# Optimization experiments

Measured on AMD Instinct MI355X. Metric: run time of the kernel, lower is better.

Reference implementation:

```python
import jax, jax.numpy as jnp
import numpy as np

B, T, S, D, V, L = 32, 128, 256, 1024, 10000, 2
EOS = 2


def setup_inputs() -> dict:
    key = jax.random.key(0)
    ks = jax.random.split(key, 12)
    s = 0.02
    targets = jax.random.randint(ks[0], (B, T), 0, V)
    targets = jnp.where(targets == EOS, 3, targets)  # decoder strips eos; keep rectangular
    return {
        'encoder_outputs': jax.random.normal(ks[1], (B, S, D), jnp.float32),
        'targets': targets,
        'emb': jax.random.normal(ks[2], (V, D)) * s,
        'W_ih': jax.random.normal(ks[3], (L, 4 * D, D)) * s,
        'W_hh': jax.random.normal(ks[4], (L, 4 * D, D)) * s,
        'b_ih': jnp.zeros((L, 4 * D)),
        'b_hh': jnp.zeros((L, 4 * D)),
        'Wconv': jax.random.normal(ks[5], (D, 3)) * s,   # Conv1d(1 -> attn_dim, k=3) kernel
        'bconv': jnp.zeros((D,)),
        'Wq': jax.random.normal(ks[6], (D, D)) * s,      # query_proj (no bias)
        'Wv': jax.random.normal(ks[7], (D, D)) * s,      # value_proj (no bias)
        'attn_bias': jax.random.uniform(ks[8], (D,), minval=-0.1, maxval=0.1),
        'fc_attn_w': jax.random.normal(ks[9], (D,)) * s, # attention score fc (D -> 1)
        'fc_attn_b': jnp.zeros(()),
        'fc1_w': jax.random.normal(ks[10], (D, 2 * D)) * s,  # Linear(2D -> D)
        'fc1_b': jnp.zeros((D,)),
        'fc2_w': jax.random.normal(ks[11], (V, D)) * s,      # Linear(D -> V)
        'fc2_b': jnp.zeros((V,)),
    }


def _forward(encoder_outputs, targets, emb, W_ih, W_hh, b_ih, b_hh, Wconv, bconv,
             Wq, Wv, attn_bias, fc_attn_w, fc_attn_b, fc1_w, fc1_b, fc2_w, fc2_b):
    b, s_len = encoder_outputs.shape[0], encoder_outputs.shape[1]
    # value_proj(encoder_outputs) is constant across decode steps
    vproj = jnp.einsum('bsd,ed->bse', encoder_outputs, Wv)
    embedded = emb[targets]                  # (B,T,D)
    xs = jnp.swapaxes(embedded, 0, 1)        # (T,B,D)
    h0 = jnp.zeros((L, b, D), embedded.dtype)
    c0 = jnp.zeros((L, b, D), embedded.dtype)
    a0 = jnp.zeros((b, s_len), embedded.dtype)  # last alignment energy starts at zero

    def step(carry, x_t):
        h, c, attn = carry
        inp = x_t
        hs, cs = [], []
        for l in range(L):  # fixed small number of LSTM layers
            gates = inp @ W_ih[l].T + b_ih[l] + h[l] @ W_hh[l].T + b_hh[l]
            i, f, g, o = jnp.split(gates, 4, axis=-1)
            c_l = jax.nn.sigmoid(f) * c[l] + jax.nn.sigmoid(i) * jnp.tanh(g)
            h_l = jax.nn.sigmoid(o) * jnp.tanh(c_l)
            hs.append(h_l); cs.append(c_l); inp = h_l
        q = inp  # decoder rnn output for this step, (B,D)
        # location_conv: Conv1d(1->D, k=3, pad=1) over last alignment
        pad = jnp.pad(attn, ((0, 0), (1, 1)))
        win = jnp.stack([pad[:, :-2], pad[:, 1:-1], pad[:, 2:]], axis=-1)  # (B,S,3)
        loc = jnp.einsum('bsk,dk->bsd', win, Wconv) + bconv
        qp = q @ Wq.T
        e = jnp.tanh(qp[:, None, :] + vproj + loc + attn_bias)  # (B,S,D)
        energy = jnp.einsum('bsd,d->bs', e, fc_attn_w) + fc_attn_b
        new_attn = jax.nn.softmax(energy, axis=-1)
        context = jnp.einsum('bs,bsd->bd', new_attn, encoder_outputs)
        hid = jnp.tanh(jnp.concatenate([q, context], axis=-1) @ fc1_w.T + fc1_b)
        logp = jax.nn.log_softmax(hid @ fc2_w.T + fc2_b, axis=-1)
        return (jnp.stack(hs), jnp.stack(cs), new_attn), logp

    _, logps = jax.lax.scan(step, (h0, c0, a0), xs)  # (T,B,V)
    return jnp.swapaxes(logps, 0, 1)                 # (B,T,V) log-probs


def reference(encoder_outputs, targets, emb, W_ih, W_hh, b_ih, b_hh, Wconv, bconv,
              Wq, Wv, attn_bias, fc_attn_w, fc_attn_b, fc1_w, fc1_b, fc2_w, fc2_b):
    return _forward(encoder_outputs, targets, emb, W_ih, W_hh, b_ih, b_hh, Wconv, bconv,
                    Wq, Wv, attn_bias, fc_attn_w, fc_attn_b, fc1_w, fc1_b, fc2_w, fc2_b)
```

## Files before the change

### kernel.cpp

```cpp
#include <hip/hip_runtime.h>
#include <stdint.h>

#define B_ 32
#define T_ 128
#define S_ 256
#define D_ 1024
#define V_ 10000

typedef unsigned short u16;
typedef unsigned char u8;
typedef unsigned long long u64;
typedef __attribute__((ext_vector_type(8))) short bf16x8;
typedef __attribute__((ext_vector_type(4))) float f32x4;
typedef __attribute__((ext_vector_type(4))) unsigned int u32x4;

__device__ __forceinline__ float bf2f(u16 u){ union { unsigned int i; float f; } v; v.i = ((unsigned int)u)<<16; return v.f; }
__device__ __forceinline__ u16 f2bf(float f){ union { float ff; unsigned int i; } v; v.ff = f; unsigned int x = v.i; return (u16)((x + 0x7fffu + ((x>>16)&1u))>>16); }
__device__ __forceinline__ float fp82f(unsigned int x){
  union { unsigned int i; float f; } v;
  v.i = ((x & 0x80u) << 24) | ((x & 0x7Fu) << 20);
  return v.f * 0x1.0p+120f;
}
__device__ __forceinline__ u8 f2fp8(float f){
  union { float ff; unsigned int i; } v;
  v.ff = fminf(fmaxf(f, -240.f), 240.f) * 0x1.0p-120f;
  unsigned int s = (v.i >> 24) & 0x80u;
  unsigned int u = v.i & 0x7FFFFFFFu;
  u += ((u >> 20) & 1u) + 0x7FFFFu;
  return (u8)(s | ((u >> 20) & 0x7Fu));
}
__device__ __forceinline__ float ftanh(float x){
  float e = __expf(2.f*x);
  return __builtin_fmaf(-2.f, __builtin_amdgcn_rcpf(1.f+e), 1.f);
}
__device__ __forceinline__ float sigm(float x){
  return __builtin_amdgcn_rcpf(1.f + __expf(-x));
}

__global__ void k_cast(const float* __restrict__ in, u16* __restrict__ out, long n){
  for (long i = (long)blockIdx.x*blockDim.x + threadIdx.x; i < n; i += (long)gridDim.x*blockDim.x)
    out[i] = f2bf(in[i]);
}

__global__ void k_cast8(const float* __restrict__ in, u8* __restrict__ out, long n){
  for (long i = (long)blockIdx.x*blockDim.x + threadIdx.x; i < n; i += (long)gridDim.x*blockDim.x)
    out[i] = f2fp8(in[i]);
}

__global__ void k_w1cat(const float* __restrict__ wih1, const float* __restrict__ whh1, u16* __restrict__ out){
  const long n = (long)4096*2048;
  for (long i = (long)blockIdx.x*blockDim.x + threadIdx.x; i < n; i += (long)gridDim.x*blockDim.x){
    int row = (int)(i >> 11), k = (int)(i & 2047);
    float v = (k < D_) ? wih1[(size_t)row*D_ + k] : whh1[(size_t)row*D_ + (k - D_)];
    out[i] = f2bf(v);
  }
}

__global__ void k_bias(const float* __restrict__ bih, const float* __restrict__ bhh,
                       const float* __restrict__ bcv, const float* __restrict__ abias,
                       const float* __restrict__ Wcv, const float* __restrict__ fcw,
                       float* __restrict__ bias0, float* __restrict__ bias1,
                       float* __restrict__ biasE, float* __restrict__ convw){
  int i = blockIdx.x*blockDim.x + threadIdx.x;
  if (i < 4096){ bias0[i] = bih[i]+bhh[i]; bias1[i] = bih[4096+i]+bhh[4096+i]; }
  if (i < 1024){
    biasE[i] = bcv[i]+abias[i];
    convw[i*4+0]=Wcv[i*3+0]; convw[i*4+1]=Wcv[i*3+1]; convw[i*4+2]=Wcv[i*3+2]; convw[i*4+3]=fcw[i];
  }
}

__global__ void k_gather(const float* __restrict__ emb, const int* __restrict__ tgt, u16* __restrict__ embA){
  int row = blockIdx.x;
  int t = row >> 5, b = row & 31;
  int e = tgt[b*T_ + t];
  const float* src = emb + (size_t)e*D_;
  u16* dst = embA + (size_t)row*D_;
  for (int d = threadIdx.x; d < D_; d += 256) dst[d] = f2bf(src[d]);
}

__device__ __forceinline__ void gld_lds(const u16* g, u16* l){
  __builtin_amdgcn_global_load_lds((const __attribute__((address_space(1))) unsigned int*)g,
                                   (__attribute__((address_space(3))) unsigned int*)l, 16, 0, 0);
}

template<int OUT_MODE, bool SWIZ>
__global__ __launch_bounds__(256) void k_gemm128(const u16* __restrict__ Am, const u16* __restrict__ Bm,
      const float* __restrict__ bias, void* __restrict__ Cout, int M, int N, int K, int lda, int ldc)
{
  __shared__ u16 As[128*32];
  __shared__ u16 Bs[128*32];
  int bm = blockIdx.y*128, bn = blockIdx.x*128;
  int tid = threadIdx.x;
  int wv = tid>>6, lane = tid&63;
  int wm = (wv>>1)*64, wn = (wv&1)*64;
  int r = lane&15, kh = lane>>4;
  f32x4 zero = {0.f,0.f,0.f,0.f};
  f32x4 acc[4][4];
  #pragma unroll
  for (int mi=0;mi<4;mi++)
    #pragma unroll
    for (int ni=0;ni<4;ni++) acc[mi][ni] = zero;

  for (int k0 = 0; k0 < K; k0 += 32){
    #pragma unroll
    for (int i=0;i<2;i++){
      int c = tid + i*256;
      int row = c>>2, ko = (c&3)*8;
      int ga = bm+row; if (ga > M-1) ga = M-1;
      gld_lds(Am + (size_t)ga*lda + k0 + ko, As + c*8);
      int gb = bn+row; if (gb > N-1) gb = N-1;
      gld_lds(Bm + (size_t)gb*K + k0 + ko, Bs + c*8);
    }
    __syncthreads();
    bf16x8 af[4], bfv[4];
    #pragma unroll
    for (int mi=0;mi<4;mi++) af[mi]  = *(const bf16x8*)(As + (wm+mi*16+r)*32 + kh*8);
    #pragma unroll
    for (int ni=0;ni<4;ni++) bfv[ni] = *(const bf16x8*)(Bs + (wn+ni*16+r)*32 + kh*8);
    #pragma unroll
    for (int mi=0;mi<4;mi++)
      #pragma unroll
      for (int ni=0;ni<4;ni++)
        acc[mi][ni] = __builtin_amdgcn_mfma_f32_16x16x32_bf16(af[mi], bfv[ni], acc[mi][ni], 0,0,0);
    __syncthreads();
  }
  #pragma unroll
  for (int mi=0;mi<4;mi++)
    #pragma unroll
    for (int ni=0;ni<4;ni++)
      #pragma unroll
      for (int rr=0;rr<4;rr++){
        int grow = bm+wm+mi*16+kh*4+rr;
        int gcol = bn+wn+ni*16+r;
        if (grow < M && gcol < N){
          float v = acc[mi][ni][rr];
          if (bias) v += bias[gcol];
          size_t orow = SWIZ ? (size_t)((grow&31)*T_ + (grow>>5)) : (size_t)grow;
          if (OUT_MODE==0)      ((float*)Cout)[orow*(size_t)ldc + gcol] = v;
          else if (OUT_MODE==1) ((u16*)Cout)[orow*(size_t)ldc + gcol] = f2bf(v);
          else if (OUT_MODE==2) ((u16*)Cout)[orow*(size_t)ldc + gcol] = f2bf(ftanh(v));
          else                  ((u8*)Cout)[orow*(size_t)ldc + gcol] = f2fp8(v);
        }
      }
}

__device__ __forceinline__ void xcd_barrier(int* barL, int it){
  asm volatile("s_waitcnt vmcnt(0)" ::: "memory");
  __syncthreads();
  if (threadIdx.x==0){
    int grp = blockIdx.x & 7;
    int* gcnt = barL + grp*32;
    int* root = barL + 256;
    int* rel  = barL + 320 + grp*32;
    int v = __hip_atomic_fetch_add(gcnt, 1, __ATOMIC_RELAXED, __HIP_MEMORY_SCOPE_AGENT);
    if (v == 32*(it+1) - 1){
      int rv = __hip_atomic_fetch_add(root, 1, __ATOMIC_RELAXED, __HIP_MEMORY_SCOPE_AGENT);
      if (rv == 8*(it+1) - 1){
        #pragma unroll
        for (int g2=0; g2<8; ++g2)
          __hip_atomic_store(barL + 320 + g2*32, it+1, __ATOMIC_RELAXED, __HIP_MEMORY_SCOPE_AGENT);
      }
    }
    while (__hip_atomic_load(rel, __ATOMIC_RELAXED, __HIP_MEMORY_SCOPE_AGENT) < it+1)
      __builtin_amdgcn_s_sleep(2);
  }
  __syncthreads();
}

__global__ __launch_bounds__(512) void k_fused(const u16* __restrict__ Whh0, const u16* __restrict__ W1cat,
    const u16* __restrict__ Wqm, const u16* __restrict__ X0, const float* __restrict__ bias1,
    const u8* __restrict__ vp8, const u8* __restrict__ enc8, const float* __restrict__ convw,
    u16* __restrict__ Hh, u16* __restrict__ qps, float* __restrict__ eng,
    u16* __restrict__ qcat, int* __restrict__ barL)
{
  __shared__ u16 W0s[16*1024];
  __shared__ u16 W1s[16*2048];
  __shared__ u16 Wqs[4*1024];
  __shared__ float gl0[8*512];
  __shared__ float gl1[8*512];
  __shared__ float glq[4*128];
  __shared__ float aw[256];
  __shared__ float red[16];
  __shared__ float cred[512];
  __shared__ u16 hb0[128];
  __shared__ u16 hb1[128];
  __shared__ u16 hbq[128];
  int bid = blockIdx.x, tid = threadIdx.x;
  int w = tid>>6, lane = tid&63, r = lane&15, kh = lane>>4;
  int batt = bid>>3, part = bid&7;
  int d0 = lane*16;
  for (int ci = tid; ci < 2048; ci += 512){
    int row = ci>>7, c = ci&127;
    int grow = (row>>2)*1024 + bid*4 + (row&3);
    bf16x8 v = *(const bf16x8*)(Whh0 + (size_t)grow*1024 + c*8);
    *(bf16x8*)(W0s + (size_t)(((row<<7) + (c ^ (row&7)))*8)) = v;
  }
  for (int ci = tid; ci < 4096; ci += 512){
    int row = ci>>8, c = ci&255;
    int grow = (row>>2)*1024 + bid*4 + (row&3);
    bf16x8 v = *(const bf16x8*)(W1cat + (size_t)grow*2048 + c*8);
    *(bf16x8*)(W1s + (size_t)(((row<<8) + (c ^ (row&7)))*8)) = v;
  }
  {
    int row = tid>>7, c = tid&127;
    bf16x8 v = *(const bf16x8*)(Wqm + (size_t)(bid*4+row)*1024 + c*8);
    *(bf16x8*)(Wqs + (size_t)(((row<<7) + (c ^ (row&7)))*8)) = v;
  }
  if (tid < 256) aw[tid] = 0.f;
  __syncthreads();
  float c0reg = 0.f, c1reg = 0.f;
  int cb = tid>>2, cj = tid&3;
  int col = bid*4 + cj;
  float b1i=0.f, b1f=0.f, b1g=0.f, b1o=0.f;
  if (tid < 128){ b1i=bias1[col]; b1f=bias1[1024+col]; b1g=bias1[2048+col]; b1o=bias1[3072+col]; }
  for (int i = 0; i <= T_+3; ++i){
    const u16* Hprev = Hh + (size_t)i*65536;
    u16* Hcur = (u16*)Hh + (size_t)(i+1)*65536;
    bool doG0 = (i < T_);
    bool doG1 = (i >= 1 && i <= T_);
    bool loadG1 = (i >= 1 && i <= T_+1);
    bool doQP = (i >= 2 && i <= T_+1);
    bool doEN = (i >= 3 && i <= T_+2);
    bool doSM = (i >= 4);
    float x_gi=0.f, x_gf=0.f, x_gg=0.f, x_go=0.f;
    if (doG0 && tid < 128){
      const u16* xr = X0 + ((size_t)i*32 + cb)*4096 + col;
      x_gi = bf2f(xr[0]); x_gf = bf2f(xr[1024]); x_gg = bf2f(xr[2048]); x_go = bf2f(xr[3072]);
    }
    bf16x8 a_g0[2][4], a_g1[2][8];
    if (doG0){
      const u16* a0 = Hprev + (size_t)r*2048 + w*128 + kh*8;
      const u16* a1 = Hprev + (size_t)(16+r)*2048 + w*128 + kh*8;
      #pragma unroll
      for (int kk=0;kk<4;kk++){ a_g0[0][kk] = *(const bf16x8*)(a0 + kk*32);
                                a_g0[1][kk] = *(const bf16x8*)(a1 + kk*32); }
    }
    if (loadG1){
      const u16* a0 = Hprev + (size_t)r*2048 + w*256 + kh*8;
      const u16* a1 = Hprev + (size_t)(16+r)*2048 + w*256 + kh*8;
      #pragma unroll
      for (int kk=0;kk<8;kk++){ a_g1[0][kk] = *(const bf16x8*)(a0 + kk*32);
                                a_g1[1][kk] = *(const bf16x8*)(a1 + kk*32); }
    }
    if (doSM){
      int t = i-4;
      float* ebuf = eng + (t&1)*8192 + batt*256;
      float e_val = -3.0e38f;
      if (tid < 256)
        e_val = __hip_atomic_load(ebuf + tid, __ATOMIC_RELAXED, __HIP_MEMORY_SCOPE_AGENT);
      float m = e_val;
      #pragma unroll
      for (int o=32;o;o>>=1) m = fmaxf(m, __shfl_xor(m,o));
      if (lane==0) red[w] = m;
      __syncthreads();
      float mx = red[0];
      #pragma unroll
      for (int i2=1;i2<8;i2++) mx = fmaxf(mx, red[i2]);
      float ex = (tid < 256) ? __expf(e_val - mx) : 0.f;
      float sl = ex;
      #pragma unroll
      for (int o=32;o;o>>=1) sl += __shfl_xor(sl,o);
      __syncthreads();
      if (lane==0) red[8+w] = sl;
      __syncthreads();
      float st = red[8]+red[9]+red[10]+red[11]+red[12]+red[13]+red[14]+red[15];
      if (tid < 256) aw[tid] = ex * __builtin_amdgcn_rcpf(st);
      __syncthreads();
      int sq = tid>>7, dt = tid&127;
      const u8* ep = enc8 + (size_t)(batt*256 + sq*64)*1024 + part*128 + dt;
      float a0=0.f,a1=0.f,a2=0.f,a3=0.f;
      #pragma unroll 4
      for (int s2=0;s2<64;s2+=4){
        a0 += aw[sq*64+s2]   * fp82f(ep[(size_t)(s2)  *1024]);
        a1 += aw[sq*64+s2+1] * fp82f(ep[(size_t)(s2+1)*1024]);
        a2 += aw[sq*64+s2+2] * fp82f(ep[(size_t)(s2+2)*1024]);
        a3 += aw[sq*64+s2+3] * fp82f(ep[(size_t)(s2+3)*1024]);
      }
      cred[tid] = a0+a1+a2+a3;
      __syncthreads();
      if (tid < 128)
        qcat[((size_t)t*32 + batt)*2048 + 1024 + part*128 + tid] =
          f2bf(cred[tid]+cred[128+tid]+cred[256+tid]+cred[384+tid]);
    }
    f32x4 acc00={0.f,0.f,0.f,0.f}, acc01={0.f,0.f,0.f,0.f};
    f32x4 acc10={0.f,0.f,0.f,0.f}, acc11={0.f,0.f,0.f,0.f};
    f32x4 accq0={0.f,0.f,0.f,0.f}, accq1={0.f,0.f,0.f,0.f};
    if (doG0){
      #pragma unroll
      for (int kk=0;kk<4;kk++){
        int c = (w<<4) + (kk<<2) + kh;
        bf16x8 bv = *(const bf16x8*)(W0s + (size_t)((((int)r<<7) + (c ^ (r&7)))*8));
        acc00 = __builtin_amdgcn_mfma_f32_16x16x32_bf16(a_g0[0][kk], bv, acc00, 0,0,0);
        acc01 = __builtin_amdgcn_mfma_f32_16x16x32_bf16(a_g0[1][kk], bv, acc01, 0,0,0);
      }
    }
    if (doG1){
      #pragma unroll
      for (int kk=0;kk<8;kk++){
        int c = (w<<5) + (kk<<2) + kh;
        bf16x8 bv = *(const bf16x8*)(W1s + (size_t)((((int)r<<8) + (c ^ (r&7)))*8));
        acc10 = __builtin_amdgcn_mfma_f32_16x16x32_bf16(a_g1[0][kk], bv, acc10, 0,0,0);
        acc11 = __builtin_amdgcn_mfma_f32_16x16x32_bf16(a_g1[1][kk], bv, acc11, 0,0,0);
      }
    }
    if (doQP && w >= 4){
      #pragma unroll
      for (int kk=0;kk<8;kk++){
        int c = ((w-4)<<5) + (kk<<2) + kh;
        int qrw = r & 3;
        bf16x8 bv = *(const bf16x8*)(Wqs + (size_t)(((qrw<<7) + (c ^ (qrw&7)))*8));
        accq0 = __builtin_amdgcn_mfma_f32_16x16x32_bf16(a_g1[0][kk], bv, accq0, 0,0,0);
        accq1 = __builtin_amdgcn_mfma_f32_16x16x32_bf16(a_g1[1][kk], bv, accq1, 0,0,0);
      }
    }
    #pragma unroll
    for (int rr=0;rr<4;rr++){
      gl0[w*512 + (kh*4+rr)*16 + r]    = acc00[rr];
      gl0[w*512 + (16+kh*4+rr)*16 + r] = acc01[rr];
      gl1[w*512 + (kh*4+rr)*16 + r]    = acc10[rr];
      gl1[w*512 + (16+kh*4+rr)*16 + r] = acc11[rr];
    }
    if (doQP && w >= 4 && r < 4){
      #pragma unroll
      for (int rr=0;rr<4;rr++){
        glq[(w-4)*128 + (kh*4+rr)*4 + r]      = accq0[rr];
        glq[(w-4)*128 + (16+kh*4+rr)*4 + r]   = accq1[rr];
      }
    }
    __syncthreads();
    if (tid < 128){
      if (doG0){
        float gi=x_gi, gf=x_gf, gg=x_gg, go=x_go;
        #pragma unroll
        for (int ww=0;ww<8;ww++){
          const float* gp = gl0 + ww*512 + cb*16 + cj;
          gi += gp[0]; gf += gp[4]; gg += gp[8]; go += gp[12];
        }
        float cn = sigm(gf)*c0reg + sigm(gi)*ftanh(gg);
        float hn = sigm(go)*ftanh(cn); c0reg = cn;
        hb0[tid] = f2bf(hn);
      }
      if (doG1){
        float gi=b1i, gf=b1f, gg=b1g, go=b1o;
        #pragma unroll
        for (int ww=0;ww<8;ww++){
          const float* gp = gl1 + ww*512 + cb*16 + cj;
          gi += gp[0]; gf += gp[4]; gg += gp[8]; go += gp[12];
        }
        float cn = sigm(gf)*c1reg + sigm(gi)*ftanh(gg);
        float hn = sigm(go)*ftanh(cn); c1reg = cn;
        hb1[tid] = f2bf(hn);
      }
      if (doQP)
        hbq[tid] = f2bf(glq[tid] + glq[128+tid] + glq[256+tid] + glq[384+tid]);
    }
    __syncthreads();
    if (tid < 32){
      union { u64 v; u16 s[4]; } pk;
      if (doG0){
        pk.s[0]=hb0[tid*4]; pk.s[1]=hb0[tid*4+1]; pk.s[2]=hb0[tid*4+2]; pk.s[3]=hb0[tid*4+3];
        __hip_atomic_store((u64*)(Hcur + (size_t)tid*2048 + bid*4), pk.v,
                           __ATOMIC_RELAXED, __HIP_MEMORY_SCOPE_AGENT);
      }
      if (doG1){
        pk.s[0]=hb1[tid*4]; pk.s[1]=hb1[tid*4+1]; pk.s[2]=hb1[tid*4+2]; pk.s[3]=hb1[tid*4+3];
        __hip_atomic_store((u64*)(Hcur + (size_t)tid*2048 + 1024 + bid*4), pk.v,
                           __ATOMIC_RELAXED, __HIP_MEMORY_SCOPE_AGENT);
        *(u64*)(qcat + ((size_t)(i-1)*32 + tid)*2048 + bid*4) = pk.v;
      }
      if (doQP){
        pk.s[0]=hbq[tid*4]; pk.s[1]=hbq[tid*4+1]; pk.s[2]=hbq[tid*4+2]; pk.s[3]=hbq[tid*4+3];
        __hip_atomic_store((u64*)(qps + ((size_t)(i-2)*32 + tid)*1024 + bid*4), pk.v,
                           __ATOMIC_RELAXED, __HIP_MEMORY_SCOPE_AGENT);
      }
    }
    if (doEN){
      int t = i-3;
      float* ebuf = eng + (t&1)*8192 + batt*256;
      const u16* qrow = qps + ((size_t)t*32 + batt)*1024 + d0;
      bf16x8 q0 = *(const bf16x8*)qrow, q1 = *(const bf16x8*)(qrow+8);
      float qf[16];
      #pragma unroll
      for (int j=0;j<16;j++) qf[j] = bf2f((u16)(j<8 ? q0[j] : q1[j-8]));
      f32x4 cw[16];
      #pragma unroll
      for (int j=0;j<16;j++) cw[j] = *(const f32x4*)(convw + (size_t)(d0+j)*4);
      #pragma unroll
      for (int ss=0; ss<4; ++ss){
        int s = part*32 + w*4 + ss;
        float am = (s>0)   ? aw[s-1] : 0.f;
        float ac =           aw[s];
        float av = (s<255) ? aw[s+1] : 0.f;
        const unsigned int* vr32 = (const unsigned int*)(vp8 + ((size_t)(batt*256+s))*1024 + d0);
        u32x4 vv4 = *(const u32x4*)vr32;
        float sum = 0.f;
        #pragma unroll
        for (int j=0;j<16;j++){
          unsigned int word = vv4[j>>2];
          float vv = fp82f((word >> ((j&3)*8)) & 0xFFu);
          float x = qf[j] + vv + am*cw[j][0] + ac*cw[j][1] + av*cw[j][2];
          sum += ftanh(x)*cw[j][3];
        }
        #pragma unroll
        for (int o=32;o;o>>=1) sum += __shfl_xor(sum, o);
        if (lane==0)
          __hip_atomic_store(ebuf + s, sum, __ATOMIC_RELAXED, __HIP_MEMORY_SCOPE_AGENT);
      }
    }
    if (i < T_+3) xcd_barrier(barL, i);
  }
}

__global__ __launch_bounds__(256) void k_logsm(float* __restrict__ out){
  int row = blockIdx.x, tid = threadIdx.x;
  float* p = out + (size_t)row*V_;
  __shared__ float red[4];
  float pv[40];
  int nv = 0;
  float mx = -3.0e38f;
  for (int v=tid; v<V_; v+=256){ float x = p[v]; pv[nv++] = x; mx = fmaxf(mx, x); }
  #pragma unroll
  for (int o=32;o;o>>=1) mx = fmaxf(mx, __shfl_xor(mx,o));
  if ((tid&63)==0) red[tid>>6]=mx;
  __syncthreads();
  mx = fmaxf(fmaxf(red[0],red[1]),fmaxf(red[2],red[3]));
  __syncthreads();
  float s = 0.f;
  for (int i=0;i<nv;i++) s += __expf(pv[i]-mx);
  #pragma unroll
  for (int o=32;o;o>>=1) s += __shfl_xor(s,o);
  if ((tid&63)==0) red[tid>>6]=s;
  __syncthreads();
  float lz = mx + __logf(red[0]+red[1]+red[2]+red[3]);
  { int i=0; for (int v=tid; v<V_; v+=256) p[v] = pv[i++] - lz; }
}

extern "C" void kernel_launch(void* const* d_in, const int* in_sizes, int n_in,
                              void* d_out, int out_size, void* d_ws, size_t ws_size,
                              hipStream_t stream)
{
  const float* enc   = (const float*)d_in[0];
  const int*   tgt   = (const int*)  d_in[1];
  const float* emb   = (const float*)d_in[2];
  const float* Wih   = (const float*)d_in[3];
  const float* Whh   = (const float*)d_in[4];
  const float* bih   = (const float*)d_in[5];
  const float* bhh   = (const float*)d_in[6];
  const float* Wcv   = (const float*)d_in[7];
  const float* bcv   = (const float*)d_in[8];
  const float* Wq    = (const float*)d_in[9];
  const float* Wvm   = (const float*)d_in[10];
  const float* abias = (const float*)d_in[11];
  const float* fcw   = (const float*)d_in[12];
  const float* fc1w  = (const float*)d_in[14];
  const float* fc1b  = (const float*)d_in[15];
  const float* fc2w  = (const float*)d_in[16];
  const float* fc2b  = (const float*)d_in[17];
  float* out = (float*)d_out;

  char* base = (char*)d_ws; size_t off = 0;
  auto A = [&](size_t nbytes)->char*{ char* q = base + off; off += (nbytes + 255) & ~(size_t)255; return q; };
  u16* enc_bf  = (u16*)A(8388608ull*2);
  u16* Wv_bf   = (u16*)A(1048576ull*2);
  u16* Wih0_bf = (u16*)A(4194304ull*2);
  u16* W1cat   = (u16*)A(8388608ull*2);
  u16* Whh0_bf = (u16*)A(4194304ull*2);
  u16* Wq_bf   = (u16*)A(1048576ull*2);
  u16* fc1w_bf = (u16*)A(2097152ull*2);
  u16* fc2w_bf = (u16*)A(10240000ull*2);
  u16* embA    = (u16*)A(4194304ull*2);
  u16* X0      = (u16*)A(16777216ull*2);
  u8*  vp8     = (u8*)A(8388608ull);
  u8*  enc8    = (u8*)A(8388608ull);
  u16* qcat    = (u16*)A(8388608ull*2);
  u16* qps     = (u16*)A(4194304ull*2);
  float* bias0 = (float*)A(4096*4);
  float* bias1 = (float*)A(4096*4);
  float* biasE = (float*)A(1024*4);
  float* convw = (float*)A(4096*4);
  float* eng   = (float*)A(2*8192*4);
  int* barL    = (int*)A(4096);
  u16* Hh      = fc2w_bf;
  u16* hid     = embA;

  hipMemsetAsync(Hh, 0, 2*65536*2, stream);
  hipMemsetAsync(barL, 0, 4096, stream);

  k_cast<<<2048,256,0,stream>>>(enc,  enc_bf,  8388608);
  k_cast8<<<2048,256,0,stream>>>(enc, enc8,    8388608);
  k_cast<<<1024,256,0,stream>>>(Wih,  Wih0_bf, 4194304);
  k_cast<<<1024,256,0,stream>>>(Whh,  Whh0_bf, 4194304);
  k_cast<<<512,256,0,stream>>>(Wq,    Wq_bf,   1048576);
  k_cast<<<512,256,0,stream>>>(Wvm,   Wv_bf,   1048576);
  k_cast<<<512,256,0,stream>>>(fc1w,  fc1w_bf, 2097152);
  k_w1cat<<<2048,256,0,stream>>>(Wih + 4194304, Whh + 4194304, W1cat);
  k_bias<<<16,256,0,stream>>>(bih, bhh, bcv, abias, Wcv, fcw, bias0, bias1, biasE, convw);
  k_gather<<<4096,256,0,stream>>>(emb, tgt, embA);

  k_gemm128<3,false><<<dim3(8,64),256,0,stream>>>(enc_bf, Wv_bf, biasE, vp8, 8192, 1024, 1024, 1024, 1024);
  k_gemm128<1,false><<<dim3(32,32),256,0,stream>>>(embA, Wih0_bf, bias0, X0, 4096, 4096, 1024, 1024, 4096);

  {
    const u16* a0 = Whh0_bf; const u16* a1 = W1cat; const u16* a2 = Wq_bf; const u16* a3 = X0;
    const float* a4 = bias1; const u8* a5 = vp8; const u8* a6 = enc8; const float* a7 = convw;
    u16* a8 = Hh; u16* a9 = qps; float* a10 = eng; u16* a11 = qcat; int* a12 = barL;
    void* args[] = {(void*)&a0,(void*)&a1,(void*)&a2,(void*)&a3,(void*)&a4,(void*)&a5,(void*)&a6,
                    (void*)&a7,(void*)&a8,(void*)&a9,(void*)&a10,(void*)&a11,(void*)&a12};
    hipError_t e = hipLaunchCooperativeKernel((const void*)k_fused, dim3(256), dim3(512), args, 0, stream);
    if (e != hipSuccess)
      k_fused<<<dim3(256),dim3(512),0,stream>>>(a0,a1,a2,a3,a4,a5,a6,a7,a8,a9,a10,a11,a12);
  }

  k_gemm128<2,false><<<dim3(8,32),256,0,stream>>>(qcat, fc1w_bf, fc1b, hid, 4096, 1024, 2048, 2048, 1024);
  k_cast<<<2048,256,0,stream>>>(fc2w, fc2w_bf, 10240000);
  k_gemm128<0,true><<<dim3(79,32),256,0,stream>>>(hid, fc2w_bf, fc2b, out, 4096, V_, 1024, 1024, V_);
  k_logsm<<<4096,256,0,stream>>>(out);
}
```

Before: 3.403 ms.

## Warp-specialize fused step: LSTM/qproj warps and attention warps run concurrently

Splits the 8 waves of each block into two roles. Waves 0-3 do the LSTM-layer and query-projection MFMAs, each handling twice the K range. Waves 4-7 do the softmax, context reduction and energy computation, interleaved between the same barriers. Hidden-state outputs are stored directly per thread instead of being staged through shared memory, and the conv weights are hoisted out of the time loop. The aim is to overlap the attention work with the matrix work on the serial recurrence path, at the cost of fewer waves per role and more registers per thread.

New measurement: 9.923 ms. 192% more time.

```diff
diff --git a/kernel.cpp b/kernel.cpp
--- a/kernel.cpp
+++ b/kernel.cpp
@@ -176,19 +176,16 @@
   __shared__ u16 W0s[16*1024];
   __shared__ u16 W1s[16*2048];
   __shared__ u16 Wqs[4*1024];
-  __shared__ float gl0[8*512];
-  __shared__ float gl1[8*512];
-  __shared__ float glq[4*128];
+  __shared__ float gl0[4*512];
+  __shared__ float gl1[4*512];
+  __shared__ float glq[2*128];
   __shared__ float aw[256];
-  __shared__ float red[16];
-  __shared__ float cred[512];
-  __shared__ u16 hb0[128];
-  __shared__ u16 hb1[128];
-  __shared__ u16 hbq[128];
+  __shared__ float red[8];
+  __shared__ float cred[256];
   int bid = blockIdx.x, tid = threadIdx.x;
   int w = tid>>6, lane = tid&63, r = lane&15, kh = lane>>4;
   int batt = bid>>3, part = bid&7;
-  int d0 = lane*16;
+  bool isATT = (w >= 4);
   for (int ci = tid; ci < 2048; ci += 512){
     int row = ci>>7, c = ci&127;
     int grow = (row>>2)*1024 + bid*4 + (row&3);
@@ -206,13 +203,19 @@
     bf16x8 v = *(const bf16x8*)(Wqm + (size_t)(bid*4+row)*1024 + c*8);
     *(bf16x8*)(Wqs + (size_t)(((row<<7) + (c ^ (row&7)))*8)) = v;
   }
-  if (tid < 256) aw[tid] = 0.f;
+  if (isATT){ int s = tid-256; aw[s] = 0.f; }
   __syncthreads();
   float c0reg = 0.f, c1reg = 0.f;
   int cb = tid>>2, cj = tid&3;
   int col = bid*4 + cj;
   float b1i=0.f, b1f=0.f, b1g=0.f, b1o=0.f;
   if (tid < 128){ b1i=bias1[col]; b1f=bias1[1024+col]; b1g=bias1[2048+col]; b1o=bias1[3072+col]; }
+  int d0 = lane*16;
+  f32x4 cw[16];
+  if (isATT){
+    #pragma unroll
+    for (int j=0;j<16;j++) cw[j] = *(const f32x4*)(convw + (size_t)(d0+j)*4);
+  }
   for (int i = 0; i <= T_+3; ++i){
     const u16* Hprev = Hh + (size_t)i*65536;
     u16* Hcur = (u16*)Hh + (size_t)(i+1)*65536;
@@ -222,189 +225,210 @@
     bool doQP = (i >= 2 && i <= T_+1);
     bool doEN = (i >= 3 && i <= T_+2);
     bool doSM = (i >= 4);
+    bf16x8 a_g0[2][8], a_g1a[2][8], a_g1b[2][8];
     float x_gi=0.f, x_gf=0.f, x_gg=0.f, x_go=0.f;
-    if (doG0 && tid < 128){
-      const u16* xr = X0 + ((size_t)i*32 + cb)*4096 + col;
-      x_gi = bf2f(xr[0]); x_gf = bf2f(xr[1024]); x_gg = bf2f(xr[2048]); x_go = bf2f(xr[3072]);
-    }
-    bf16x8 a_g0[2][4], a_g1[2][8];
-    if (doG0){
-      const u16* a0 = Hprev + (size_t)r*2048 + w*128 + kh*8;
-      const u16* a1 = Hprev + (size_t)(16+r)*2048 + w*128 + kh*8;
-      #pragma unroll
-      for (int kk=0;kk<4;kk++){ a_g0[0][kk] = *(const bf16x8*)(a0 + kk*32);
-                                a_g0[1][kk] = *(const bf16x8*)(a1 + kk*32); }
-    }
-    if (loadG1){
-      const u16* a0 = Hprev + (size_t)r*2048 + w*256 + kh*8;
-      const u16* a1 = Hprev + (size_t)(16+r)*2048 + w*256 + kh*8;
-      #pragma unroll
-      for (int kk=0;kk<8;kk++){ a_g1[0][kk] = *(const bf16x8*)(a0 + kk*32);
-                                a_g1[1][kk] = *(const bf16x8*)(a1 + kk*32); }
-    }
-    if (doSM){
-      int t = i-4;
-      float* ebuf = eng + (t&1)*8192 + batt*256;
-      float e_val = -3.0e38f;
-      if (tid < 256)
-        e_val = __hip_atomic_load(ebuf + tid, __ATOMIC_RELAXED, __HIP_MEMORY_SCOPE_AGENT);
-      float m = e_val;
-      #pragma unroll
-      for (int o=32;o;o>>=1) m = fmaxf(m, __shfl_xor(m,o));
-      if (lane==0) red[w] = m;
-      __syncthreads();
-      float mx = red[0];
-      #pragma unroll
-      for (int i2=1;i2<8;i2++) mx = fmaxf(mx, red[i2]);
-      float ex = (tid < 256) ? __expf(e_val - mx) : 0.f;
-      float sl = ex;
-      #pragma unroll
-      for (int o=32;o;o>>=1) sl += __shfl_xor(sl,o);
-      __syncthreads();
-      if (lane==0) red[8+w] = sl;
-      __syncthreads();
-      float st = red[8]+red[9]+red[10]+red[11]+red[12]+red[13]+red[14]+red[15];
-      if (tid < 256) aw[tid] = ex * __builtin_amdgcn_rcpf(st);
-      __syncthreads();
-      int sq = tid>>7, dt = tid&127;
-      const u8* ep = enc8 + (size_t)(batt*256 + sq*64)*1024 + part*128 + dt;
-      float a0=0.f,a1=0.f,a2=0.f,a3=0.f;
-      #pragma unroll 4
-      for (int s2=0;s2<64;s2+=4){
-        a0 += aw[sq*64+s2]   * fp82f(ep[(size_t)(s2)  *1024]);
-        a1 += aw[sq*64+s2+1] * fp82f(ep[(size_t)(s2+1)*1024]);
-        a2 += aw[sq*64+s2+2] * fp82f(ep[(size_t)(s2+2)*1024]);
-        a3 += aw[sq*64+s2+3] * fp82f(ep[(size_t)(s2+3)*1024]);
-      }
-      cred[tid] = a0+a1+a2+a3;
-      __syncthreads();
-      if (tid < 128)
-        qcat[((size_t)t*32 + batt)*2048 + 1024 + part*128 + tid] =
-          f2bf(cred[tid]+cred[128+tid]+cred[256+tid]+cred[384+tid]);
-    }
+    float e_val=0.f, ex=0.f;
+    if (!isATT){
+      if (doG0){
+        const u16* a0 = Hprev + (size_t)r*2048 + w*256 + kh*8;
+        const u16* a1 = Hprev + (size_t)(16+r)*2048 + w*256 + kh*8;
+        #pragma unroll
+        for (int kk=0;kk<8;kk++){ a_g0[0][kk] = *(const bf16x8*)(a0 + kk*32);
+                                  a_g0[1][kk] = *(const bf16x8*)(a1 + kk*32); }
+      }
+      if (loadG1){
+        const u16* a0 = Hprev + (size_t)r*2048 + w*512 + kh*8;
+        const u16* a1 = Hprev + (size_t)(16+r)*2048 + w*512 + kh*8;
+        #pragma unroll
+        for (int kk=0;kk<8;kk++){ a_g1a[0][kk] = *(const bf16x8*)(a0 + kk*32);
+                                  a_g1a[1][kk] = *(const bf16x8*)(a1 + kk*32); }
+        #pragma unroll
+        for (int kk=0;kk<8;kk++){ a_g1b[0][kk] = *(const bf16x8*)(a0 + 256 + kk*32);
+                                  a_g1b[1][kk] = *(const bf16x8*)(a1 + 256 + kk*32); }
+      }
+      if (doG0 && tid < 128){
+        const u16* xr = X0 + ((size_t)i*32 + cb)*4096 + col;
+        x_gi = bf2f(xr[0]); x_gf = bf2f(xr[1024]); x_gg = bf2f(xr[2048]); x_go = bf2f(xr[3072]);
+      }
+    } else {
+      if (doSM){
+        int t = i-4;
+        float* ebuf = eng + (t&1)*8192 + batt*256;
+        int s = tid-256;
+        e_val = __hip_atomic_load(ebuf + s, __ATOMIC_RELAXED, __HIP_MEMORY_SCOPE_AGENT);
+        float m = e_val;
+        #pragma unroll
+        for (int o=32;o;o>>=1) m = fmaxf(m, __shfl_xor(m,o));
+        if (lane==0) red[w-4] = m;
+      }
+    }
+    __syncthreads();
     f32x4 acc00={0.f,0.f,0.f,0.f}, acc01={0.f,0.f,0.f,0.f};
     f32x4 acc10={0.f,0.f,0.f,0.f}, acc11={0.f,0.f,0.f,0.f};
     f32x4 accq0={0.f,0.f,0.f,0.f}, accq1={0.f,0.f,0.f,0.f};
-    if (doG0){
-      #pragma unroll
-      for (int kk=0;kk<4;kk++){
-        int c = (w<<4) + (kk<<2) + kh;
-        bf16x8 bv = *(const bf16x8*)(W0s + (size_t)((((int)r<<7) + (c ^ (r&7)))*8));
-        acc00 = __builtin_amdgcn_mfma_f32_16x16x32_bf16(a_g0[0][kk], bv, acc00, 0,0,0);
-        acc01 = __builtin_amdgcn_mfma_f32_16x16x32_bf16(a_g0[1][kk], bv, acc01, 0,0,0);
-      }
-    }
-    if (doG1){
-      #pragma unroll
-      for (int kk=0;kk<8;kk++){
-        int c = (w<<5) + (kk<<2) + kh;
-        bf16x8 bv = *(const bf16x8*)(W1s + (size_t)((((int)r<<8) + (c ^ (r&7)))*8));
-        acc10 = __builtin_amdgcn_mfma_f32_16x16x32_bf16(a_g1[0][kk], bv, acc10, 0,0,0);
-        acc11 = __builtin_amdgcn_mfma_f32_16x16x32_bf16(a_g1[1][kk], bv, acc11, 0,0,0);
-      }
-    }
-    if (doQP && w >= 4){
-      #pragma unroll
-      for (int kk=0;kk<8;kk++){
-        int c = ((w-4)<<5) + (kk<<2) + kh;
+    if (!isATT){
+      if (doG0){
+        #pragma unroll
+        for (int kk=0;kk<8;kk++){
+          int c = (w<<5) + (kk<<2) + kh;
+          bf16x8 bv = *(const bf16x8*)(W0s + (size_t)((((int)r<<7) + (c ^ (r&7)))*8));
+          acc00 = __builtin_amdgcn_mfma_f32_16x16x32_bf16(a_g0[0][kk], bv, acc00, 0,0,0);
+          acc01 = __builtin_amdgcn_mfma_f32_16x16x32_bf16(a_g0[1][kk], bv, acc01, 0,0,0);
+        }
+      }
+      if (doG1){
+        #pragma unroll
+        for (int kk=0;kk<8;kk++){
+          int c = (w<<6) + (kk<<2) + kh;
+          bf16x8 bv = *(const bf16x8*)(W1s + (size_t)((((int)r<<8) + (c ^ (r&7)))*8));
+          acc10 = __builtin_amdgcn_mfma_f32_16x16x32_bf16(a_g1a[0][kk], bv, acc10, 0,0,0);
+          acc11 = __builtin_amdgcn_mfma_f32_16x16x32_bf16(a_g1a[1][kk], bv, acc11, 0,0,0);
+        }
+      }
+    } else {
+      if (doSM){
+        float mx = fmaxf(fmaxf(red[0],red[1]),fmaxf(red[2],red[3]));
+        ex = __expf(e_val - mx);
+        float sl = ex;
+        #pragma unroll
+        for (int o=32;o;o>>=1) sl += __shfl_xor(sl,o);
+        if (lane==0) red[4+(w-4)] = sl;
+      }
+    }
+    __syncthreads();
+    if (!isATT){
+      if (doG1){
+        #pragma unroll
+        for (int kk=0;kk<8;kk++){
+          int c = (w<<6) + 32 + (kk<<2) + kh;
+          bf16x8 bv = *(const bf16x8*)(W1s + (size_t)((((int)r<<8) + (c ^ (r&7)))*8));
+          acc10 = __builtin_amdgcn_mfma_f32_16x16x32_bf16(a_g1b[0][kk], bv, acc10, 0,0,0);
+          acc11 = __builtin_amdgcn_mfma_f32_16x16x32_bf16(a_g1b[1][kk], bv, acc11, 0,0,0);
+        }
+      }
+      if (doQP && w >= 2){
         int qrw = r & 3;
-        bf16x8 bv = *(const bf16x8*)(Wqs + (size_t)(((qrw<<7) + (c ^ (qrw&7)))*8));
-        accq0 = __builtin_amdgcn_mfma_f32_16x16x32_bf16(a_g1[0][kk], bv, accq0, 0,0,0);
-        accq1 = __builtin_amdgcn_mfma_f32_16x16x32_bf16(a_g1[1][kk], bv, accq1, 0,0,0);
-      }
-    }
-    #pragma unroll
-    for (int rr=0;rr<4;rr++){
-      gl0[w*512 + (kh*4+rr)*16 + r]    = acc00[rr];
-      gl0[w*512 + (16+kh*4+rr)*16 + r] = acc01[rr];
-      gl1[w*512 + (kh*4+rr)*16 + r]    = acc10[rr];
-      gl1[w*512 + (16+kh*4+rr)*16 + r] = acc11[rr];
-    }
-    if (doQP && w >= 4 && r < 4){
+        #pragma unroll
+        for (int kk=0;kk<8;kk++){
+          int c = ((w-2)<<6) + (kk<<2) + kh;
+          bf16x8 bv = *(const bf16x8*)(Wqs + (size_t)(((qrw<<7) + (c ^ (qrw&7)))*8));
+          accq0 = __builtin_amdgcn_mfma_f32_16x16x32_bf16(a_g1a[0][kk], bv, accq0, 0,0,0);
+          accq1 = __builtin_amdgcn_mfma_f32_16x16x32_bf16(a_g1a[1][kk], bv, accq1, 0,0,0);
+        }
+        #pragma unroll
+        for (int kk=0;kk<8;kk++){
+          int c = ((w-2)<<6) + 32 + (kk<<2) + kh;
+          bf16x8 bv = *(const bf16x8*)(Wqs + (size_t)(((qrw<<7) + (c ^ (qrw&7)))*8));
+          accq0 = __builtin_amdgcn_mfma_f32_16x16x32_bf16(a_g1b[0][kk], bv, accq0, 0,0,0);
+          accq1 = __builtin_amdgcn_mfma_f32_16x16x32_bf16(a_g1b[1][kk], bv, accq1, 0,0,0);
+        }
+      }
       #pragma unroll
       for (int rr=0;rr<4;rr++){
-        glq[(w-4)*128 + (kh*4+rr)*4 + r]      = accq0[rr];
-        glq[(w-4)*128 + (16+kh*4+rr)*4 + r]   = accq1[rr];
+        gl0[w*512 + (kh*4+rr)*16 + r]    = acc00[rr];
+        gl0[w*512 + (16+kh*4+rr)*16 + r] = acc01[rr];
+        gl1[w*512 + (kh*4+rr)*16 + r]    = acc10[rr];
+        gl1[w*512 + (16+kh*4+rr)*16 + r] = acc11[rr];
+      }
+      if (doQP && w >= 2 && r < 4){
+        #pragma unroll
+        for (int rr=0;rr<4;rr++){
+          glq[(w-2)*128 + (kh*4+rr)*4 + r]    = accq0[rr];
+          glq[(w-2)*128 + (16+kh*4+rr)*4 + r] = accq1[rr];
+        }
+      }
+    } else {
+      if (doSM){
+        float st = red[4]+red[5]+red[6]+red[7];
+        aw[tid-256] = ex * __builtin_amdgcn_rcpf(st);
       }
     }
     __syncthreads();
-    if (tid < 128){
-      if (doG0){
-        float gi=x_gi, gf=x_gf, gg=x_gg, go=x_go;
-        #pragma unroll
-        for (int ww=0;ww<8;ww++){
-          const float* gp = gl0 + ww*512 + cb*16 + cj;
-          gi += gp[0]; gf += gp[4]; gg += gp[8]; go += gp[12];
-        }
-        float cn = sigm(gf)*c0reg + sigm(gi)*ftanh(gg);
-        float hn = sigm(go)*ftanh(cn); c0reg = cn;
-        hb0[tid] = f2bf(hn);
-      }
-      if (doG1){
-        float gi=b1i, gf=b1f, gg=b1g, go=b1o;
-        #pragma unroll
-        for (int ww=0;ww<8;ww++){
-          const float* gp = gl1 + ww*512 + cb*16 + cj;
-          gi += gp[0]; gf += gp[4]; gg += gp[8]; go += gp[12];
-        }
-        float cn = sigm(gf)*c1reg + sigm(gi)*ftanh(gg);
-        float hn = sigm(go)*ftanh(cn); c1reg = cn;
-        hb1[tid] = f2bf(hn);
-      }
-      if (doQP)
-        hbq[tid] = f2bf(glq[tid] + glq[128+tid] + glq[256+tid] + glq[384+tid]);
+    if (!isATT){
+      if (tid < 128){
+        if (doG0){
+          float gi=x_gi, gf=x_gf, gg=x_gg, go=x_go;
+          #pragma unroll
+          for (int ww=0;ww<4;ww++){
+            const float* gp = gl0 + ww*512 + cb*16 + cj;
+            gi += gp[0]; gf += gp[4]; gg += gp[8]; go += gp[12];
+          }
+          float cn = sigm(gf)*c0reg + sigm(gi)*ftanh(gg);
+          float hn = sigm(go)*ftanh(cn); c0reg = cn;
+          __hip_atomic_store(Hcur + (size_t)cb*2048 + col, f2bf(hn),
+                             __ATOMIC_RELAXED, __HIP_MEMORY_SCOPE_AGENT);
+        }
+        if (doG1){
+          float gi=b1i, gf=b1f, gg=b1g, go=b1o;
+          #pragma unroll
+          for (int ww=0;ww<4;ww++){
+            const float* gp = gl1 + ww*512 + cb*16 + cj;
+            gi += gp[0]; gf += gp[4]; gg += gp[8]; go += gp[12];
+          }
+          float cn = sigm(gf)*c1reg + sigm(gi)*ftanh(gg);
+          float hn = sigm(go)*ftanh(cn); c1reg = cn;
+          u16 hb = f2bf(hn);
+          __hip_atomic_store(Hcur + (size_t)cb*2048 + 1024 + col, hb,
+                             __ATOMIC_RELAXED, __HIP_MEMORY_SCOPE_AGENT);
+          qcat[((size_t)(i-1)*32 + cb)*2048 + col] = hb;
+        }
+        if (doQP){
+          float hq = glq[cb*4+cj] + glq[128 + cb*4+cj];
+          __hip_atomic_store(qps + ((size_t)(i-2)*32 + cb)*1024 + col, f2bf(hq),
+                             __ATOMIC_RELAXED, __HIP_MEMORY_SCOPE_AGENT);
+        }
+      }
+    } else {
+      if (doSM){
+        int ct = tid-256, sq = ct>>7, dt = ct&127;
+        const u8* ep = enc8 + (size_t)(batt*256 + sq*128)*1024 + part*128 + dt;
+        float a0=0.f,a1=0.f,a2=0.f,a3=0.f;
+        #pragma unroll 4
+        for (int s2=0;s2<128;s2+=4){
+          a0 += aw[sq*128+s2]   * fp82f(ep[(size_t)(s2)  *1024]);
+          a1 += aw[sq*128+s2+1] * fp82f(ep[(size_t)(s2+1)*1024]);
+          a2 += aw[sq*128+s2+2] * fp82f(ep[(size_t)(s2+2)*1024]);
+          a3 += aw[sq*128+s2+3] * fp82f(ep[(size_t)(s2+3)*1024]);
+        }
+        cred[ct] = a0+a1+a2+a3;
+      }
     }
     __syncthreads();
-    if (tid < 32){
-      union { u64 v; u16 s[4]; } pk;
-      if (doG0){
-        pk.s[0]=hb0[tid*4]; pk.s[1]=hb0[tid*4+1]; pk.s[2]=hb0[tid*4+2]; pk.s[3]=hb0[tid*4+3];
-        __hip_atomic_store((u64*)(Hcur + (size_t)tid*2048 + bid*4), pk.v,
-                           __ATOMIC_RELAXED, __HIP_MEMORY_SCOPE_AGENT);
-      }
-      if (doG1){
-        pk.s[0]=hb1[tid*4]; pk.s[1]=hb1[tid*4+1]; pk.s[2]=hb1[tid*4+2]; pk.s[3]=hb1[tid*4+3];
-        __hip_atomic_store((u64*)(Hcur + (size_t)tid*2048 + 1024 + bid*4), pk.v,
-                           __ATOMIC_RELAXED, __HIP_MEMORY_SCOPE_AGENT);
-        *(u64*)(qcat + ((size_t)(i-1)*32 + tid)*2048 + bid*4) = pk.v;
-      }
-      if (doQP){
-        pk.s[0]=hbq[tid*4]; pk.s[1]=hbq[tid*4+1]; pk.s[2]=hbq[tid*4+2]; pk.s[3]=hbq[tid*4+3];
-        __hip_atomic_store((u64*)(qps + ((size_t)(i-2)*32 + tid)*1024 + bid*4), pk.v,
-                           __ATOMIC_RELAXED, __HIP_MEMORY_SCOPE_AGENT);
-      }
-    }
-    if (doEN){
-      int t = i-3;
-      float* ebuf = eng + (t&1)*8192 + batt*256;
-      const u16* qrow = qps + ((size_t)t*32 + batt)*1024 + d0;
-      bf16x8 q0 = *(const bf16x8*)qrow, q1 = *(const bf16x8*)(qrow+8);
-      float qf[16];
-      #pragma unroll
-      for (int j=0;j<16;j++) qf[j] = bf2f((u16)(j<8 ? q0[j] : q1[j-8]));
-      f32x4 cw[16];
-      #pragma unroll
-      for (int j=0;j<16;j++) cw[j] = *(const f32x4*)(convw + (size_t)(d0+j)*4);
-      #pragma unroll
-      for (int ss=0; ss<4; ++ss){
-        int s = part*32 + w*4 + ss;
-        float am = (s>0)   ? aw[s-1] : 0.f;
-        float ac =           aw[s];
-        float av = (s<255) ? aw[s+1] : 0.f;
-        const unsigned int* vr32 = (const unsigned int*)(vp8 + ((size_t)(batt*256+s))*1024 + d0);
-        u32x4 vv4 = *(const u32x4*)vr32;
-        float sum = 0.f;
-        #pragma unroll
-        for (int j=0;j<16;j++){
-          unsigned int word = vv4[j>>2];
-          float vv = fp82f((word >> ((j&3)*8)) & 0xFFu);
-          float x = qf[j] + vv + am*cw[j][0] + ac*cw[j][1] + av*cw[j][2];
-          sum += ftanh(x)*cw[j][3];
-        }
-        #pragma unroll
-        for (int o=32;o;o>>=1) sum += __shfl_xor(sum, o);
-        if (lane==0)
-          __hip_atomic_store(ebuf + s, sum, __ATOMIC_RELAXED, __HIP_MEMORY_SCOPE_AGENT);
+    if (isATT){
+      if (doSM){
+        int ct = tid-256, t = i-4;
+        if (ct < 128)
+          qcat[((size_t)t*32 + batt)*2048 + 1024 + part*128 + ct] =
+            f2bf(cred[ct] + cred[128+ct]);
+      }
+      if (doEN){
+        int t = i-3;
+        float* ebuf = eng + (t&1)*8192 + batt*256;
+        const u16* qrow = qps + ((size_t)t*32 + batt)*1024 + d0;
+        bf16x8 q0 = *(const bf16x8*)qrow, q1 = *(const bf16x8*)(qrow+8);
+        float qf[16];
+        #pragma unroll
+        for (int j=0;j<16;j++) qf[j] = bf2f((u16)(j<8 ? q0[j] : q1[j-8]));
+        #pragma unroll
+        for (int ss=0; ss<8; ++ss){
+          int s = part*32 + (w-4)*8 + ss;
+          float am = (s>0)   ? aw[s-1] : 0.f;
+          float ac =           aw[s];
+          float av = (s<255) ? aw[s+1] : 0.f;
+          const u32x4 vv4 = *(const u32x4*)(vp8 + ((size_t)(batt*256+s))*1024 + d0);
+          float sum = 0.f;
+          #pragma unroll
+          for (int j=0;j<16;j++){
+            unsigned int word = vv4[j>>2];
+            float vv = fp82f((word >> ((j&3)*8)) & 0xFFu);
+            float x = qf[j] + vv + am*cw[j][0] + ac*cw[j][1] + av*cw[j][2];
+            sum += ftanh(x)*cw[j][3];
+          }
+          #pragma unroll
+          for (int o=32;o;o>>=1) sum += __shfl_xor(sum, o);
+          if (lane==0)
+            __hip_atomic_store(ebuf + s, sum, __ATOMIC_RELAXED, __HIP_MEMORY_SCOPE_AGENT);
+        }
       }
     }
     if (i < T_+3) xcd_barrier(barL, i);
```
